# Performance work log

Hardware: AMD Instinct MI355X
Metric: run time of the kernel (lower is better)

Reference implementation:

```python
import jax, jax.numpy as jnp
import numpy as np

N, D, E = 16384, 1024, 65536
HID, H1, NCLS = 512, 8, 2


def _glorot(key, shape):
    fan = shape[0] + shape[-1]
    return jax.random.normal(key, shape, jnp.float32) * np.sqrt(2.0 / fan)


def setup_inputs() -> dict:
    key = jax.random.key(0)
    ks = jax.random.split(key, 12)
    return {
        "x": jax.random.normal(ks[0], (N, D), jnp.float32),
        "edge_index": jax.random.randint(ks[1], (2, E), 0, N, dtype=jnp.int32),
        # layer 1: GATConv((-1,-1), 512, heads=8, concat=True)
        "W1_src": _glorot(ks[2], (D, H1 * HID)),
        "W1_dst": _glorot(ks[3], (D, H1 * HID)),
        "att1_src": _glorot(ks[4], (H1, HID)),
        "att1_dst": _glorot(ks[5], (H1, HID)),
        "b1": jnp.zeros((H1 * HID,), jnp.float32),
        # layer 2: GATConv((-1,-1), 2, heads=1, concat=False)
        "W2_src": _glorot(ks[6], (H1 * HID, NCLS)),
        "W2_dst": _glorot(ks[7], (H1 * HID, NCLS)),
        "att2_src": _glorot(ks[8], (1, NCLS)),
        "att2_dst": _glorot(ks[9], (1, NCLS)),
        "b2": jnp.zeros((NCLS,), jnp.float32),
    }


def gat_layer(x, src, dst, Ws, Wd, a_s, a_d, b, heads, ch, concat):
    n = x.shape[0]
    hs = (x @ Ws).reshape(n, heads, ch)  # source-transformed feats [N,H,C]
    hd = (x @ Wd).reshape(n, heads, ch)  # dest-transformed feats  [N,H,C]
    al_s = jnp.einsum("nhc,hc->nh", hs, a_s)  # [N,H]
    al_d = jnp.einsum("nhc,hc->nh", hd, a_d)
    logits = jax.nn.leaky_relu(al_s[src] + al_d[dst], 0.2)  # [E,H]
    # segment softmax over incoming edges of each destination node
    m = jax.ops.segment_max(logits, dst, num_segments=n)
    m = jnp.where(jnp.isfinite(m), m, 0.0)
    e = jnp.exp(logits - m[dst])
    denom = jax.ops.segment_sum(e, dst, num_segments=n)
    alpha = e / (denom[dst] + 1e-16)  # [E,H]
    msg = hs[src] * alpha[:, :, None]  # [E,H,C]
    out = jax.ops.segment_sum(msg, dst, num_segments=n)  # [N,H,C]
    out = out.reshape(n, heads * ch) if concat else out.mean(axis=1)
    return out + b


def reference(x, edge_index, W1_src, W1_dst, att1_src, att1_dst, b1,
              W2_src, W2_dst, att2_src, att2_dst, b2):
    n = x.shape[0]
    # PyG GATConv adds self-loops by default
    loops = jnp.arange(n, dtype=edge_index.dtype)
    src = jnp.concatenate([edge_index[0], loops])
    dst = jnp.concatenate([edge_index[1], loops])
    h = gat_layer(x, src, dst, W1_src, W1_dst, att1_src, att1_dst, b1,
                  H1, HID, concat=True)  # [N, 4096]
    out = gat_layer(h, src, dst, W2_src, W2_dst, att2_src, att2_dst, b2,
                    1, NCLS, concat=False)  # [N, 2]
    return out
```

## Files before the change

### kernel.cpp

```cpp
#include <hip/hip_runtime.h>
#include <cstdint>
#include <cstddef>

#define DEV __device__ __forceinline__

typedef __attribute__((ext_vector_type(8))) short bf16x8;
typedef __attribute__((ext_vector_type(4))) float f32x4;

constexpr int N_  = 16384;
constexpr int D_  = 1024;
constexpr int E_  = 65536;
constexpr int ET_ = E_ + N_;
constexpr int H_  = 8;
constexpr int C_  = 512;
constexpr int F_  = 4096;
constexpr int ZS_ = 48;

DEV unsigned short f2bf(float f){
  unsigned u = __float_as_uint(f);
  unsigned r = u + 0x7FFFu + ((u >> 16) & 1u);
  return (unsigned short)(r >> 16);
}
DEV float lrelu(float x){ return x >= 0.f ? x : 0.2f * x; }
DEV float waveSum(float v){
  #pragma unroll
  for (int o = 32; o > 0; o >>= 1) v += __shfl_xor(v, o);
  return v;
}
DEV int eSRC(const int* ei, int e){ return e < E_ ? ei[e]      : e - E_; }
DEV int eDST(const int* ei, int e){ return e < E_ ? ei[E_ + e] : e - E_; }

__global__ void init_all(float* __restrict__ den1, float* __restrict__ den2,
                         float* __restrict__ s0a, float* __restrict__ s1a,
                         float* __restrict__ sda, unsigned* __restrict__ vbz){
  int i = blockIdx.x * blockDim.x + threadIdx.x;
  if (i < N_ * H_) den1[i] = 0.f;
  if (i < N_){ den2[i] = 0.f; s0a[i] = 0.f; s1a[i] = 0.f; sda[i] = 0.f; }
  if (i < 3 * 32 * 64 * 8 / 2) vbz[i] = 0u;
}

__global__ void build_wd2(const float* __restrict__ W2d, const float* __restrict__ a2d,
                          float* __restrict__ wd2){
  int k = blockIdx.x * blockDim.x + threadIdx.x;
  if (k < F_) wd2[k] = W2d[k * 2] * a2d[0] + W2d[k * 2 + 1] * a2d[1];
}

__global__ __launch_bounds__(256) void build_cb(const float* __restrict__ b1,
                                                const float* __restrict__ W2s,
                                                const float* __restrict__ wd2,
                                                float* __restrict__ cb){
  __shared__ float red[3][4];
  int t = threadIdx.x, w = t >> 6, lane = t & 63;
  float p0 = 0.f, p1 = 0.f, pd = 0.f;
  for (int k = t; k < F_; k += 256){
    float b = b1[k];
    p0 += b * W2s[k * 2]; p1 += b * W2s[k * 2 + 1]; pd += b * wd2[k];
  }
  p0 = waveSum(p0); p1 = waveSum(p1); pd = waveSum(pd);
  if (lane == 0){ red[0][w] = p0; red[1][w] = p1; red[2][w] = pd; }
  __syncthreads();
  if (t == 0){
    cb[0] = red[0][0] + red[0][1] + red[0][2] + red[0][3];
    cb[1] = red[1][0] + red[1][1] + red[1][2] + red[1][3];
    cb[2] = red[2][0] + red[2][1] + red[2][2] + red[2][3];
  }
}

__global__ __launch_bounds__(256) void build_V(
    const float* __restrict__ W1s, const float* __restrict__ W1d,
    const float* __restrict__ a1s, const float* __restrict__ a1d,
    const float* __restrict__ W2s, const float* __restrict__ wd2,
    unsigned short* __restrict__ Vb){
  int t = threadIdx.x;
  int id = blockIdx.x * 4 + (t >> 6);
  int lane = t & 63;
  int d = id >> 3, h = id & 7;
  float sa = 0.f, sb = 0.f, s0 = 0.f, s1 = 0.f, sd = 0.f;
  #pragma unroll
  for (int i = 0; i < C_ / 64; i++){
    int c = i * 64 + lane;
    int gc = h * C_ + c;
    float ws = W1s[(size_t)d * F_ + gc];
    float wdv = W1d[(size_t)d * F_ + gc];
    sa += ws * a1s[gc]; sb += wdv * a1d[gc];
    float2 w2 = *reinterpret_cast<const float2*>(W2s + (size_t)gc * 2);
    s0 += ws * w2.x; s1 += ws * w2.y; sd += ws * wd2[gc];
  }
  sa = waveSum(sa); sb = waveSum(sb);
  s0 = waveSum(s0); s1 = waveSum(s1); sd = waveSum(sd);
  if (lane == 0){
    int kc = d >> 5, ks = (d >> 3) & 3, ii = d & 7;
    auto put = [&](int jj, float v){
      int tt = jj >> 4, j = jj & 15;
      Vb[((size_t)(tt * 32 + kc) * 64 + ks * 16 + j) * 8 + ii] = f2bf(v);
    };
    put(h, sa); put(8 + h, sb); put(16 + h, s0); put(24 + h, s1); put(32 + h, sd);
  }
}

__global__ __launch_bounds__(64) void node_mfma(const float* __restrict__ X,
                                                const unsigned short* __restrict__ Vb,
                                                float* __restrict__ Z){
  int lane = threadIdx.x;
  int n0 = blockIdx.x * 16;
  int row = lane & 15, ks = lane >> 4;
  f32x4 ac0 = {0.f,0.f,0.f,0.f}, ac1 = ac0, ac2 = ac0;
  const float* xp = X + (size_t)(n0 + row) * D_ + ks * 8;
  #pragma unroll 2
  for (int kc = 0; kc < 32; kc++){
    float4 xa = *reinterpret_cast<const float4*>(xp + kc * 32);
    float4 xb = *reinterpret_cast<const float4*>(xp + kc * 32 + 4);
    bf16x8 a;
    a[0] = (short)f2bf(xa.x); a[1] = (short)f2bf(xa.y);
    a[2] = (short)f2bf(xa.z); a[3] = (short)f2bf(xa.w);
    a[4] = (short)f2bf(xb.x); a[5] = (short)f2bf(xb.y);
    a[6] = (short)f2bf(xb.z); a[7] = (short)f2bf(xb.w);
    bf16x8 b0 = *reinterpret_cast<const bf16x8*>(&Vb[((size_t)( 0 + kc) * 64 + lane) * 8]);
    bf16x8 b1 = *reinterpret_cast<const bf16x8*>(&Vb[((size_t)(32 + kc) * 64 + lane) * 8]);
    bf16x8 b2 = *reinterpret_cast<const bf16x8*>(&Vb[((size_t)(64 + kc) * 64 + lane) * 8]);
    ac0 = __builtin_amdgcn_mfma_f32_16x16x32_bf16(a, b0, ac0, 0, 0, 0);
    ac1 = __builtin_amdgcn_mfma_f32_16x16x32_bf16(a, b1, ac1, 0, 0, 0);
    ac2 = __builtin_amdgcn_mfma_f32_16x16x32_bf16(a, b2, ac2, 0, 0, 0);
  }
  #pragma unroll
  for (int r = 0; r < 4; r++){
    int n = n0 + ks * 4 + r;
    Z[(size_t)n * ZS_ +  0 + row] = ac0[r];
    Z[(size_t)n * ZS_ + 16 + row] = ac1[r];
    Z[(size_t)n * ZS_ + 32 + row] = ac2[r];
  }
}

__global__ void edge_exp1(const int* __restrict__ ei, const float* __restrict__ Z,
                          float* __restrict__ expv, float* __restrict__ den1){
  int t = blockIdx.x * blockDim.x + threadIdx.x;
  if (t >= ET_ * H_) return;
  int e = t >> 3, h = t & 7;
  int s = eSRC(ei, e), d = eDST(ei, e);
  float lg = lrelu(Z[(size_t)s * ZS_ + h] + Z[(size_t)d * ZS_ + 8 + h]);
  float ev = expf(lg);
  expv[e * 8 + h] = ev;
  atomicAdd(&den1[d * 8 + h], ev);
}

__global__ void agg_z(const int* __restrict__ ei, const float* __restrict__ Z,
                      const float* __restrict__ expv, const float* __restrict__ den1,
                      float* __restrict__ s0a, float* __restrict__ s1a,
                      float* __restrict__ sda){
  int e = blockIdx.x * blockDim.x + threadIdx.x;
  if (e >= ET_) return;
  int s = eSRC(ei, e), d = eDST(ei, e);
  float4 ev0 = *reinterpret_cast<const float4*>(expv + e * 8);
  float4 ev1 = *reinterpret_cast<const float4*>(expv + e * 8 + 4);
  float4 dn0 = *reinterpret_cast<const float4*>(den1 + d * 8);
  float4 dn1 = *reinterpret_cast<const float4*>(den1 + d * 8 + 4);
  float al[8];
  al[0] = ev0.x / (dn0.x + 1e-16f); al[1] = ev0.y / (dn0.y + 1e-16f);
  al[2] = ev0.z / (dn0.z + 1e-16f); al[3] = ev0.w / (dn0.w + 1e-16f);
  al[4] = ev1.x / (dn1.x + 1e-16f); al[5] = ev1.y / (dn1.y + 1e-16f);
  al[6] = ev1.z / (dn1.z + 1e-16f); al[7] = ev1.w / (dn1.w + 1e-16f);
  const float* zp = Z + (size_t)s * ZS_;
  float4 z0a = *reinterpret_cast<const float4*>(zp + 16);
  float4 z0b = *reinterpret_cast<const float4*>(zp + 20);
  float4 z1a = *reinterpret_cast<const float4*>(zp + 24);
  float4 z1b = *reinterpret_cast<const float4*>(zp + 28);
  float4 zda = *reinterpret_cast<const float4*>(zp + 32);
  float4 zdb = *reinterpret_cast<const float4*>(zp + 36);
  float p0 = al[0]*z0a.x + al[1]*z0a.y + al[2]*z0a.z + al[3]*z0a.w
           + al[4]*z0b.x + al[5]*z0b.y + al[6]*z0b.z + al[7]*z0b.w;
  float p1 = al[0]*z1a.x + al[1]*z1a.y + al[2]*z1a.z + al[3]*z1a.w
           + al[4]*z1b.x + al[5]*z1b.y + al[6]*z1b.z + al[7]*z1b.w;
  float pd = al[0]*zda.x + al[1]*zda.y + al[2]*zda.z + al[3]*zda.w
           + al[4]*zdb.x + al[5]*zdb.y + al[6]*zdb.z + al[7]*zdb.w;
  atomicAdd(&s0a[d], p0);
  atomicAdd(&s1a[d], p1);
  atomicAdd(&sda[d], pd);
}

__global__ void finalize_l2(const float* __restrict__ s0a, const float* __restrict__ s1a,
                            const float* __restrict__ sda, const float* __restrict__ cb,
                            const float* __restrict__ a2s, const float* __restrict__ b2,
                            float* __restrict__ s0b, float* __restrict__ s1b,
                            float* __restrict__ als2, float* __restrict__ ald2,
                            float* __restrict__ out){
  int n = blockIdx.x * blockDim.x + threadIdx.x;
  if (n >= N_) return;
  float v0 = s0a[n] + cb[0], v1 = s1a[n] + cb[1], vd = sda[n] + cb[2];
  s0b[n] = v0; s1b[n] = v1;
  als2[n] = v0 * a2s[0] + v1 * a2s[1];
  ald2[n] = vd;
  out[2 * n] = b2[0]; out[2 * n + 1] = b2[1];
}

__global__ void edge_exp2(const int* __restrict__ ei, const float* __restrict__ als2,
                          const float* __restrict__ ald2, float* __restrict__ expv2,
                          float* __restrict__ den2){
  int e = blockIdx.x * blockDim.x + threadIdx.x;
  if (e >= ET_) return;
  int s = eSRC(ei, e), d = eDST(ei, e);
  float ev = expf(lrelu(als2[s] + ald2[d]));
  expv2[e] = ev;
  atomicAdd(&den2[d], ev);
}

__global__ void aggregate2(const int* __restrict__ ei, const float* __restrict__ expv2,
                           const float* __restrict__ den2, const float* __restrict__ s0b,
                           const float* __restrict__ s1b, float* __restrict__ out){
  int e = blockIdx.x * blockDim.x + threadIdx.x;
  if (e >= ET_) return;
  int s = eSRC(ei, e), d = eDST(ei, e);
  float a = expv2[e] / (den2[d] + 1e-16f);
  atomicAdd(&out[2 * d],     a * s0b[s]);
  atomicAdd(&out[2 * d + 1], a * s1b[s]);
}

extern "C" void kernel_launch(void* const* d_in, const int* in_sizes, int n_in,
                              void* d_out, int out_size, void* d_ws, size_t ws_size,
                              hipStream_t stream){
  const float* x   = (const float*)d_in[0];
  const int*   ei  = (const int*)  d_in[1];
  const float* W1s = (const float*)d_in[2];
  const float* W1d = (const float*)d_in[3];
  const float* a1s = (const float*)d_in[4];
  const float* a1d = (const float*)d_in[5];
  const float* b1  = (const float*)d_in[6];
  const float* W2s = (const float*)d_in[7];
  const float* W2d = (const float*)d_in[8];
  const float* a2s = (const float*)d_in[9];
  const float* a2d = (const float*)d_in[10];
  const float* b2  = (const float*)d_in[11];
  float* out = (float*)d_out;

  char* p = (char*)d_ws;
  auto alloc = [&](size_t bytes) -> void* {
    void* r = (void*)p;
    p += (bytes + 255) & ~(size_t)255;
    return r;
  };
  unsigned short* Vb = (unsigned short*)alloc((size_t)3 * 32 * 64 * 8 * 2);
  float* wd2   = (float*)alloc((size_t)F_ * 4);
  float* cb    = (float*)alloc(256);
  float* Z     = (float*)alloc((size_t)N_ * ZS_ * 4);
  float* expv1 = (float*)alloc((size_t)ET_ * H_ * 4);
  float* den1  = (float*)alloc((size_t)N_ * H_ * 4);
  float* s0a   = (float*)alloc((size_t)N_ * 4);
  float* s1a   = (float*)alloc((size_t)N_ * 4);
  float* sda   = (float*)alloc((size_t)N_ * 4);
  float* s0b   = (float*)alloc((size_t)N_ * 4);
  float* s1b   = (float*)alloc((size_t)N_ * 4);
  float* als2  = (float*)alloc((size_t)N_ * 4);
  float* ald2  = (float*)alloc((size_t)N_ * 4);
  float* den2  = (float*)alloc((size_t)N_ * 4);
  float* expv2 = (float*)alloc((size_t)ET_ * 4);

  init_all<<<dim3(N_ * H_ / 256), dim3(256), 0, stream>>>(den1, den2, s0a, s1a, sda,
                                                          (unsigned*)Vb);
  build_wd2<<<dim3(F_ / 256), dim3(256), 0, stream>>>(W2d, a2d, wd2);
  build_cb<<<dim3(1), dim3(256), 0, stream>>>(b1, W2s, wd2, cb);
  build_V<<<dim3(D_ * H_ / 4), dim3(256), 0, stream>>>(W1s, W1d, a1s, a1d, W2s, wd2, Vb);

  node_mfma<<<dim3(N_ / 16), dim3(64), 0, stream>>>(x, Vb, Z);

  edge_exp1<<<dim3(ET_ * H_ / 256), dim3(256), 0, stream>>>(ei, Z, expv1, den1);
  agg_z<<<dim3(ET_ / 256), dim3(256), 0, stream>>>(ei, Z, expv1, den1, s0a, s1a, sda);

  finalize_l2<<<dim3(N_ / 256), dim3(256), 0, stream>>>(s0a, s1a, sda, cb, a2s, b2,
                                                        s0b, s1b, als2, ald2, out);
  edge_exp2<<<dim3(ET_ / 256), dim3(256), 0, stream>>>(ei, als2, ald2, expv2, den2);
  aggregate2<<<dim3(ET_ / 256), dim3(256), 0, stream>>>(ei, expv2, den2, s0b, s1b, out);
}
```

Baseline: 80.85 us.

## Merge small setup kernels, split node GEMM K across blocks, drop finalize pass

Folds the wd2 build into the zeroing kernel, merges the cb reduction into build_V as an extra block, and removes finalize_l2 by computing the layer-2 logits and messages on the fly in edge_exp2 and aggregate2. Z, den1, den2 and the s*a buffers are now laid out contiguously and zeroed with a single uint4 memset-style pass. node_mfma splits its K loop over two blocks in grid y and accumulates into Z with atomics, doubling the block count to raise occupancy. The cost is extra atomic traffic on Z, non-deterministic summation order, and some redundant per-edge recomputation.

```diff
diff --git a/kernel.cpp b/kernel.cpp
--- a/kernel.cpp
+++ b/kernel.cpp
@@ -15,6 +15,7 @@
 constexpr int C_  = 512;
 constexpr int F_  = 4096;
 constexpr int ZS_ = 48;
+constexpr int KSPLIT = 2;
 
 DEV unsigned short f2bf(float f){
   unsigned u = __float_as_uint(f);
@@ -30,48 +31,39 @@
 DEV int eSRC(const int* ei, int e){ return e < E_ ? ei[e]      : e - E_; }
 DEV int eDST(const int* ei, int e){ return e < E_ ? ei[E_ + e] : e - E_; }
 
-__global__ void init_all(float* __restrict__ den1, float* __restrict__ den2,
-                         float* __restrict__ s0a, float* __restrict__ s1a,
-                         float* __restrict__ sda, unsigned* __restrict__ vbz){
+__global__ void init_all(uint4* __restrict__ zr, int n16,
+                         const float* __restrict__ W2d, const float* __restrict__ a2d,
+                         float* __restrict__ wd2){
   int i = blockIdx.x * blockDim.x + threadIdx.x;
-  if (i < N_ * H_) den1[i] = 0.f;
-  if (i < N_){ den2[i] = 0.f; s0a[i] = 0.f; s1a[i] = 0.f; sda[i] = 0.f; }
-  if (i < 3 * 32 * 64 * 8 / 2) vbz[i] = 0u;
-}
-
-__global__ void build_wd2(const float* __restrict__ W2d, const float* __restrict__ a2d,
-                          float* __restrict__ wd2){
-  int k = blockIdx.x * blockDim.x + threadIdx.x;
-  if (k < F_) wd2[k] = W2d[k * 2] * a2d[0] + W2d[k * 2 + 1] * a2d[1];
-}
-
-__global__ __launch_bounds__(256) void build_cb(const float* __restrict__ b1,
-                                                const float* __restrict__ W2s,
-                                                const float* __restrict__ wd2,
-                                                float* __restrict__ cb){
-  __shared__ float red[3][4];
-  int t = threadIdx.x, w = t >> 6, lane = t & 63;
-  float p0 = 0.f, p1 = 0.f, pd = 0.f;
-  for (int k = t; k < F_; k += 256){
-    float b = b1[k];
-    p0 += b * W2s[k * 2]; p1 += b * W2s[k * 2 + 1]; pd += b * wd2[k];
-  }
-  p0 = waveSum(p0); p1 = waveSum(p1); pd = waveSum(pd);
-  if (lane == 0){ red[0][w] = p0; red[1][w] = p1; red[2][w] = pd; }
-  __syncthreads();
-  if (t == 0){
-    cb[0] = red[0][0] + red[0][1] + red[0][2] + red[0][3];
-    cb[1] = red[1][0] + red[1][1] + red[1][2] + red[1][3];
-    cb[2] = red[2][0] + red[2][1] + red[2][2] + red[2][3];
-  }
-}
-
-__global__ __launch_bounds__(256) void build_V(
+  if (i < n16){ uint4 z = {0u,0u,0u,0u}; zr[i] = z; }
+  if (i < F_) wd2[i] = W2d[i * 2] * a2d[0] + W2d[i * 2 + 1] * a2d[1];
+}
+
+__global__ __launch_bounds__(256) void build_Vcb(
     const float* __restrict__ W1s, const float* __restrict__ W1d,
     const float* __restrict__ a1s, const float* __restrict__ a1d,
     const float* __restrict__ W2s, const float* __restrict__ wd2,
-    unsigned short* __restrict__ Vb){
+    const float* __restrict__ b1,
+    unsigned short* __restrict__ Vb, float* __restrict__ cb){
   int t = threadIdx.x;
+  if (blockIdx.x == D_ * H_ / 4){
+    __shared__ float red[3][4];
+    int w = t >> 6, lane = t & 63;
+    float p0 = 0.f, p1 = 0.f, pd = 0.f;
+    for (int k = t; k < F_; k += 256){
+      float b = b1[k];
+      p0 += b * W2s[k * 2]; p1 += b * W2s[k * 2 + 1]; pd += b * wd2[k];
+    }
+    p0 = waveSum(p0); p1 = waveSum(p1); pd = waveSum(pd);
+    if (lane == 0){ red[0][w] = p0; red[1][w] = p1; red[2][w] = pd; }
+    __syncthreads();
+    if (t == 0){
+      cb[0] = red[0][0] + red[0][1] + red[0][2] + red[0][3];
+      cb[1] = red[1][0] + red[1][1] + red[1][2] + red[1][3];
+      cb[2] = red[2][0] + red[2][1] + red[2][2] + red[2][3];
+    }
+    return;
+  }
   int id = blockIdx.x * 4 + (t >> 6);
   int lane = t & 63;
   int d = id >> 3, h = id & 7;
@@ -80,7 +72,7 @@
   for (int i = 0; i < C_ / 64; i++){
     int c = i * 64 + lane;
     int gc = h * C_ + c;
-    float ws = W1s[(size_t)d * F_ + gc];
+    float ws  = W1s[(size_t)d * F_ + gc];
     float wdv = W1d[(size_t)d * F_ + gc];
     sa += ws * a1s[gc]; sb += wdv * a1d[gc];
     float2 w2 = *reinterpret_cast<const float2*>(W2s + (size_t)gc * 2);
@@ -103,11 +95,14 @@
                                                 float* __restrict__ Z){
   int lane = threadIdx.x;
   int n0 = blockIdx.x * 16;
+  int kh = blockIdx.y;
   int row = lane & 15, ks = lane >> 4;
   f32x4 ac0 = {0.f,0.f,0.f,0.f}, ac1 = ac0, ac2 = ac0;
   const float* xp = X + (size_t)(n0 + row) * D_ + ks * 8;
+  constexpr int KC = 32 / KSPLIT;
   #pragma unroll 2
-  for (int kc = 0; kc < 32; kc++){
+  for (int kk = 0; kk < KC; kk++){
+    int kc = kh * KC + kk;
     float4 xa = *reinterpret_cast<const float4*>(xp + kc * 32);
     float4 xb = *reinterpret_cast<const float4*>(xp + kc * 32 + 4);
     bf16x8 a;
@@ -125,9 +120,9 @@
   #pragma unroll
   for (int r = 0; r < 4; r++){
     int n = n0 + ks * 4 + r;
-    Z[(size_t)n * ZS_ +  0 + row] = ac0[r];
-    Z[(size_t)n * ZS_ + 16 + row] = ac1[r];
-    Z[(size_t)n * ZS_ + 32 + row] = ac2[r];
+    atomicAdd(&Z[(size_t)n * ZS_ +  0 + row], ac0[r]);
+    atomicAdd(&Z[(size_t)n * ZS_ + 16 + row], ac1[r]);
+    atomicAdd(&Z[(size_t)n * ZS_ + 32 + row], ac2[r]);
   }
 }
 
@@ -177,41 +172,33 @@
   atomicAdd(&sda[d], pd);
 }
 
-__global__ void finalize_l2(const float* __restrict__ s0a, const float* __restrict__ s1a,
-                            const float* __restrict__ sda, const float* __restrict__ cb,
-                            const float* __restrict__ a2s, const float* __restrict__ b2,
-                            float* __restrict__ s0b, float* __restrict__ s1b,
-                            float* __restrict__ als2, float* __restrict__ ald2,
-                            float* __restrict__ out){
-  int n = blockIdx.x * blockDim.x + threadIdx.x;
-  if (n >= N_) return;
-  float v0 = s0a[n] + cb[0], v1 = s1a[n] + cb[1], vd = sda[n] + cb[2];
-  s0b[n] = v0; s1b[n] = v1;
-  als2[n] = v0 * a2s[0] + v1 * a2s[1];
-  ald2[n] = vd;
-  out[2 * n] = b2[0]; out[2 * n + 1] = b2[1];
-}
-
-__global__ void edge_exp2(const int* __restrict__ ei, const float* __restrict__ als2,
-                          const float* __restrict__ ald2, float* __restrict__ expv2,
-                          float* __restrict__ den2){
+__global__ void edge_exp2(const int* __restrict__ ei, const float* __restrict__ s0a,
+                          const float* __restrict__ s1a, const float* __restrict__ sda,
+                          const float* __restrict__ cb, const float* __restrict__ a2s,
+                          const float* __restrict__ b2,
+                          float* __restrict__ expv2, float* __restrict__ den2,
+                          float* __restrict__ out){
   int e = blockIdx.x * blockDim.x + threadIdx.x;
   if (e >= ET_) return;
   int s = eSRC(ei, e), d = eDST(ei, e);
-  float ev = expf(lrelu(als2[s] + ald2[d]));
+  float als = (s0a[s] + cb[0]) * a2s[0] + (s1a[s] + cb[1]) * a2s[1];
+  float ald = sda[d] + cb[2];
+  float ev = expf(lrelu(als + ald));
   expv2[e] = ev;
   atomicAdd(&den2[d], ev);
+  if (e < N_){ out[2 * e] = b2[0]; out[2 * e + 1] = b2[1]; }
 }
 
 __global__ void aggregate2(const int* __restrict__ ei, const float* __restrict__ expv2,
-                           const float* __restrict__ den2, const float* __restrict__ s0b,
-                           const float* __restrict__ s1b, float* __restrict__ out){
+                           const float* __restrict__ den2, const float* __restrict__ s0a,
+                           const float* __restrict__ s1a, const float* __restrict__ cb,
+                           float* __restrict__ out){
   int e = blockIdx.x * blockDim.x + threadIdx.x;
   if (e >= ET_) return;
   int s = eSRC(ei, e), d = eDST(ei, e);
   float a = expv2[e] / (den2[d] + 1e-16f);
-  atomicAdd(&out[2 * d],     a * s0b[s]);
-  atomicAdd(&out[2 * d + 1], a * s1b[s]);
+  atomicAdd(&out[2 * d],     a * (s0a[s] + cb[0]));
+  atomicAdd(&out[2 * d + 1], a * (s1a[s] + cb[1]));
 }
 
 extern "C" void kernel_launch(void* const* d_in, const int* in_sizes, int n_in,
@@ -238,34 +225,28 @@
     return r;
   };
   unsigned short* Vb = (unsigned short*)alloc((size_t)3 * 32 * 64 * 8 * 2);
-  float* wd2   = (float*)alloc((size_t)F_ * 4);
-  float* cb    = (float*)alloc(256);
   float* Z     = (float*)alloc((size_t)N_ * ZS_ * 4);
-  float* expv1 = (float*)alloc((size_t)ET_ * H_ * 4);
   float* den1  = (float*)alloc((size_t)N_ * H_ * 4);
+  float* den2  = (float*)alloc((size_t)N_ * 4);
   float* s0a   = (float*)alloc((size_t)N_ * 4);
   float* s1a   = (float*)alloc((size_t)N_ * 4);
   float* sda   = (float*)alloc((size_t)N_ * 4);
-  float* s0b   = (float*)alloc((size_t)N_ * 4);
-  float* s1b   = (float*)alloc((size_t)N_ * 4);
-  float* als2  = (float*)alloc((size_t)N_ * 4);
-  float* ald2  = (float*)alloc((size_t)N_ * 4);
-  float* den2  = (float*)alloc((size_t)N_ * 4);
+  float* wd2   = (float*)alloc((size_t)F_ * 4);
+  float* cb    = (float*)alloc(256);
+  float* expv1 = (float*)alloc((size_t)ET_ * H_ * 4);
   float* expv2 = (float*)alloc((size_t)ET_ * 4);
 
-  init_all<<<dim3(N_ * H_ / 256), dim3(256), 0, stream>>>(den1, den2, s0a, s1a, sda,
-                                                          (unsigned*)Vb);
-  build_wd2<<<dim3(F_ / 256), dim3(256), 0, stream>>>(W2d, a2d, wd2);
-  build_cb<<<dim3(1), dim3(256), 0, stream>>>(b1, W2s, wd2, cb);
-  build_V<<<dim3(D_ * H_ / 4), dim3(256), 0, stream>>>(W1s, W1d, a1s, a1d, W2s, wd2, Vb);
-
-  node_mfma<<<dim3(N_ / 16), dim3(64), 0, stream>>>(x, Vb, Z);
-
+  size_t zrBytes = (size_t)((char*)wd2 - (char*)Vb);
+  int n16 = (int)(zrBytes / 16);
+  int g1 = (int)((((n16 > F_) ? n16 : F_) + 255) / 256);
+
+  init_all<<<dim3(g1), dim3(256), 0, stream>>>((uint4*)Vb, n16, W2d, a2d, wd2);
+  build_Vcb<<<dim3(D_ * H_ / 4 + 1), dim3(256), 0, stream>>>(W1s, W1d, a1s, a1d,
+                                                             W2s, wd2, b1, Vb, cb);
+  node_mfma<<<dim3(N_ / 16, KSPLIT), dim3(64), 0, stream>>>(x, Vb, Z);
   edge_exp1<<<dim3(ET_ * H_ / 256), dim3(256), 0, stream>>>(ei, Z, expv1, den1);
   agg_z<<<dim3(ET_ / 256), dim3(256), 0, stream>>>(ei, Z, expv1, den1, s0a, s1a, sda);
-
-  finalize_l2<<<dim3(N_ / 256), dim3(256), 0, stream>>>(s0a, s1a, sda, cb, a2s, b2,
-                                                        s0b, s1b, als2, ald2, out);
-  edge_exp2<<<dim3(ET_ / 256), dim3(256), 0, stream>>>(ei, als2, ald2, expv2, den2);
-  aggregate2<<<dim3(ET_ / 256), dim3(256), 0, stream>>>(ei, expv2, den2, s0b, s1b, out);
-}
+  edge_exp2<<<dim3(ET_ / 256), dim3(256), 0, stream>>>(ei, s0a, s1a, sda, cb, a2s, b2,
+                                                       expv2, den2, out);
+  aggregate2<<<dim3(ET_ / 256), dim3(256), 0, stream>>>(ei, expv2, den2, s0a, s1a, cb, out);
+}
```

After: 74.77 us. -7.5%, faster.
